# Performance work log

Measured on AMD Instinct MI355X. Metric: run time of the kernel, lower is better.

The kernel has to match this reference:

```python
import jax, jax.numpy as jnp
import numpy as np

D_M, D_K, D_V, HEADS = 1024, 64, 64, 16
B, S = 2, 2048


def setup_inputs() -> dict:
    key = jax.random.key(0)
    ks = jax.random.split(key, 5)
    x = jax.random.normal(ks[0], (B, S, D_M), dtype=jnp.float32)
    # per-head projection weights (original deep-copies one rand init per head;
    # we give each head independent weights, matching the per-head param structure)
    Wk = jax.random.uniform(ks[1], (HEADS, D_M, D_K), dtype=jnp.float32)
    Wq = jax.random.uniform(ks[2], (HEADS, D_M, D_K), dtype=jnp.float32)
    Wv = jax.random.uniform(ks[3], (HEADS, D_M, D_V), dtype=jnp.float32)
    Wo = jax.random.uniform(ks[4], (HEADS * D_V, D_M), dtype=jnp.float32)
    return {"x": x, "Wk": Wk, "Wq": Wq, "Wv": Wv, "Wo": Wo}


def reference(x, Wk, Wq, Wv, Wo):
    # per-head QKV projections, batched over heads: [B,H,S,d]
    q = jnp.einsum("bsm,hmk->bhsk", x, Wq)
    k = jnp.einsum("bsm,hmk->bhsk", x, Wk)
    v = jnp.einsum("bsm,hmv->bhsv", x, Wv)
    scale = 1.0 / jnp.sqrt(jnp.asarray(q.shape[-1], dtype=q.dtype))
    scores = jnp.einsum("bhsk,bhtk->bhst", q, k) * scale  # [B,H,S,S]
    attn = jax.nn.softmax(scores, axis=-1)
    ctx = jnp.einsum("bhst,bhtv->bhsv", attn, v)  # [B,H,S,d_v]
    # concat heads -> [B,S,H*d_v], then output projection
    ctx = jnp.transpose(ctx, (0, 2, 1, 3)).reshape(x.shape[0], x.shape[1], -1)
    return jnp.einsum("bsc,cm->bsm", ctx, Wo)
```

## Files before the change

kernel.cpp:

```cpp
#include <hip/hip_runtime.h>
#include <hip/hip_bf16.h>
#include <stdint.h>

#define DM   1024
#define DKV  64
#define HEADS 16
#define BATCH 2
#define SEQ  2048
#define BS   (BATCH*SEQ)
#define BHD  (BATCH*HEADS)

typedef __attribute__((ext_vector_type(8))) short bf16x8;
typedef __attribute__((ext_vector_type(4))) short bf16x4;
typedef __attribute__((ext_vector_type(4))) float f32x4;

__device__ inline unsigned fb(float f) { union { float f; unsigned u; } v; v.f = f; return v.u; }

__device__ inline unsigned short bf16_rtn(float f) {
  unsigned u = fb(f);
  unsigned r = u + 0x7fffu + ((u >> 16) & 1u);
  return (unsigned short)(r >> 16);
}
__device__ inline float bf16_to_f(unsigned short h) {
  union { unsigned u; float f; } v; v.u = ((unsigned)h) << 16; return v.f;
}
__device__ inline void split_bf16(float x, unsigned short& hi, unsigned short& lo) {
  hi = bf16_rtn(x);
  lo = bf16_rtn(x - bf16_to_f(hi));
}
__device__ inline unsigned pack2_bf16(float lo_elem, float hi_elem) {
  return __builtin_amdgcn_perm(fb(hi_elem) + 0x8000u, fb(lo_elem) + 0x8000u, 0x07060302u);
}

__device__ inline float fast_exp2(float x) {
#if __has_builtin(__builtin_amdgcn_exp2f)
  return __builtin_amdgcn_exp2f(x);
#else
  return exp2f(x);
#endif
}

__device__ inline f32x4 mfma16x16x16_bf16(bf16x4 a, bf16x4 b, f32x4 c) {
#if __has_builtin(__builtin_amdgcn_mfma_f32_16x16x16bf16_1k)
  return __builtin_amdgcn_mfma_f32_16x16x16bf16_1k(a, b, c, 0, 0, 0);
#else
  asm volatile("v_mfma_f32_16x16x16_bf16 %0, %1, %2, %0" : "+v"(c) : "v"(a), "v"(b));
  return c;
#endif
}

__device__ inline void stage16(const unsigned short* g, unsigned short* lds_base, int lane) {
#if __has_builtin(__builtin_amdgcn_global_load_lds)
  __builtin_amdgcn_global_load_lds((__attribute__((address_space(1))) void*)(g),
                                   (__attribute__((address_space(3))) void*)(lds_base),
                                   16, 0, 0);
#else
  *(bf16x8*)(lds_base + lane * 8) = *(const bf16x8*)g;
#endif
}

__device__ inline int swz(int row, int chunk) {
  return row * 64 + (((chunk ^ (row & 7)) & 7) << 3);
}

__global__ void cvt_x_split(const float* __restrict__ x,
                            unsigned short* __restrict__ xh, unsigned short* __restrict__ xl) {
  int i = (blockIdx.x * 256 + threadIdx.x) * 8;
  bf16x8 oh, ol;
  #pragma unroll
  for (int j = 0; j < 8; ++j) {
    unsigned short hi, lo;
    split_bf16(x[i + j], hi, lo);
    oh[j] = (short)hi; ol[j] = (short)lo;
  }
  *(bf16x8*)(xh + i) = oh;
  *(bf16x8*)(xl + i) = ol;
}

__global__ void pack_qkv_split(const float* __restrict__ Wq, const float* __restrict__ Wk,
                               const float* __restrict__ Wv,
                               unsigned short* __restrict__ Wh, unsigned short* __restrict__ Wl) {
  __shared__ float tile[64][65];
  int bid = blockIdx.x;
  int p = bid >> 8, h = (bid >> 4) & 15, mt = bid & 15;
  const float* W = (p == 0) ? Wq : (p == 1) ? Wk : Wv;
  const float* src = W + (size_t)h * (DM * DKV);
  int t = threadIdx.x;
  int m0 = mt * 64;
  #pragma unroll
  for (int pass = 0; pass < 16; ++pass) {
    int row = pass * 4 + (t >> 6), col = t & 63;
    tile[row][col] = src[(size_t)(m0 + row) * DKV + col];
  }
  __syncthreads();
  int cbase = p * 1024 + h * 64;
  #pragma unroll
  for (int pass = 0; pass < 16; ++pass) {
    int krow = pass * 4 + (t >> 6), mcol = t & 63;
    unsigned short hi, lo;
    split_bf16(tile[mcol][krow], hi, lo);
    size_t idx = (size_t)(cbase + krow) * DM + m0 + mcol;
    Wh[idx] = hi; Wl[idx] = lo;
  }
}

__global__ void pack_wo(const float* __restrict__ Wo, unsigned short* __restrict__ WoT) {
  __shared__ float tile[64][65];
  int ib = blockIdx.x >> 4, jb = blockIdx.x & 15;
  int t = threadIdx.x;
  #pragma unroll
  for (int pass = 0; pass < 16; ++pass) {
    int row = pass * 4 + (t >> 6), col = t & 63;
    tile[row][col] = Wo[(size_t)(ib * 64 + row) * DM + jb * 64 + col];
  }
  __syncthreads();
  #pragma unroll
  for (int pass = 0; pass < 16; ++pass) {
    int a = pass * 4 + (t >> 6), b = t & 63;
    WoT[(size_t)(jb * 64 + a) * DM + ib * 64 + b] = bf16_rtn(tile[b][a]);
  }
}

__global__ __launch_bounds__(256, 2)
void gemm_qk(const unsigned short* __restrict__ Ah, const unsigned short* __restrict__ Al,
             const unsigned short* __restrict__ Bh, const unsigned short* __restrict__ Bl,
             unsigned short* __restrict__ Qh, unsigned short* __restrict__ Ql,
             unsigned short* __restrict__ Kh, unsigned short* __restrict__ Kl) {
  __shared__ unsigned short AsH[128 * 32], AsL[128 * 32];
  __shared__ unsigned short BsH[128 * 32], BsL[128 * 32];
  const int tid = threadIdx.x;
  const int w = tid >> 6, lane = tid & 63;
  const int quad = lane >> 4, l16 = lane & 15;
  const int wm = w >> 1, wn = w & 1;
  const int bn = blockIdx.x, bm = blockIdx.y;

  f32x4 acc[4][4];
  #pragma unroll
  for (int i = 0; i < 4; ++i)
    #pragma unroll
    for (int j = 0; j < 4; ++j) acc[i][j] = (f32x4){0.f, 0.f, 0.f, 0.f};

  const int r4 = lane >> 2, c4 = lane & 3;
  const size_t offA = (size_t)(bm * 128 + w * 32 + r4) * DM + c4 * 8;
  const size_t offB = (size_t)(bn * 128 + w * 32 + r4) * DM + c4 * 8;
  unsigned short* lAh0 = AsH + (w * 32) * 32;      unsigned short* lAh1 = AsH + (w * 32 + 16) * 32;
  unsigned short* lAl0 = AsL + (w * 32) * 32;      unsigned short* lAl1 = AsL + (w * 32 + 16) * 32;
  unsigned short* lBh0 = BsH + (w * 32) * 32;      unsigned short* lBh1 = BsH + (w * 32 + 16) * 32;
  unsigned short* lBl0 = BsL + (w * 32) * 32;      unsigned short* lBl1 = BsL + (w * 32 + 16) * 32;

  for (int kk = 0; kk < DM / 32; ++kk) {
    stage16(Ah + offA + kk * 32,           lAh0, lane);
    stage16(Ah + offA + kk * 32 + 16 * DM, lAh1, lane);
    stage16(Al + offA + kk * 32,           lAl0, lane);
    stage16(Al + offA + kk * 32 + 16 * DM, lAl1, lane);
    stage16(Bh + offB + kk * 32,           lBh0, lane);
    stage16(Bh + offB + kk * 32 + 16 * DM, lBh1, lane);
    stage16(Bl + offB + kk * 32,           lBl0, lane);
    stage16(Bl + offB + kk * 32 + 16 * DM, lBl1, lane);
    asm volatile("s_waitcnt vmcnt(0)" ::: "memory");
    __syncthreads();
    bf16x8 afh[4], afl[4], bfh[4], bfl[4];
    #pragma unroll
    for (int mt = 0; mt < 4; ++mt) {
      afh[mt] = *(const bf16x8*)(AsH + (wm * 64 + mt * 16 + l16) * 32 + quad * 8);
      afl[mt] = *(const bf16x8*)(AsL + (wm * 64 + mt * 16 + l16) * 32 + quad * 8);
    }
    #pragma unroll
    for (int nt = 0; nt < 4; ++nt) {
      bfh[nt] = *(const bf16x8*)(BsH + (wn * 64 + nt * 16 + l16) * 32 + quad * 8);
      bfl[nt] = *(const bf16x8*)(BsL + (wn * 64 + nt * 16 + l16) * 32 + quad * 8);
    }
    #pragma unroll
    for (int mt = 0; mt < 4; ++mt)
      #pragma unroll
      for (int nt = 0; nt < 4; ++nt) {
        acc[mt][nt] = __builtin_amdgcn_mfma_f32_16x16x32_bf16(afh[mt], bfh[nt], acc[mt][nt], 0, 0, 0);
        acc[mt][nt] = __builtin_amdgcn_mfma_f32_16x16x32_bf16(afh[mt], bfl[nt], acc[mt][nt], 0, 0, 0);
        acc[mt][nt] = __builtin_amdgcn_mfma_f32_16x16x32_bf16(afl[mt], bfh[nt], acc[mt][nt], 0, 0, 0);
      }
    __syncthreads();
  }

  const float SCL = 0.18033688011112042f;
  #pragma unroll
  for (int mt = 0; mt < 4; ++mt) {
    int m_g = bm * 128 + wm * 64 + mt * 16 + quad * 4;
    #pragma unroll
    for (int nt = 0; nt < 4; ++nt) {
      int n_g = bn * 128 + wn * 64 + nt * 16 + l16;
      int p = n_g >> 10, h = (n_g >> 6) & 15, k = n_g & 63;
      #pragma unroll
      for (int r = 0; r < 4; ++r) {
        int row = m_g + r;
        int b = row >> 11, s = row & 2047;
        int bh = b * HEADS + h;
        float v = acc[mt][nt][r];
        size_t idx = ((size_t)(bh * SEQ + s)) * DKV + k;
        unsigned short hi, lo;
        if (p == 0) {
          split_bf16(v * SCL, hi, lo);
          Qh[idx] = hi; Ql[idx] = lo;
        } else {
          split_bf16(v, hi, lo);
          Kh[idx] = hi; Kl[idx] = lo;
        }
      }
    }
  }
}

__global__ __launch_bounds__(256, 2)
void gemm_v(const unsigned short* __restrict__ A, const unsigned short* __restrict__ Bt,
            unsigned short* __restrict__ Vt) {
  __shared__ unsigned short As[128 * 32];
  __shared__ unsigned short Bs[128 * 32];
  const int tid = threadIdx.x;
  const int w = tid >> 6, lane = tid & 63;
  const int quad = lane >> 4, l16 = lane & 15;
  const int wm = w >> 1, wn = w & 1;
  const int bn = blockIdx.x, bm = blockIdx.y;

  f32x4 acc[4][4];
  #pragma unroll
  for (int i = 0; i < 4; ++i)
    #pragma unroll
    for (int j = 0; j < 4; ++j) acc[i][j] = (f32x4){0.f, 0.f, 0.f, 0.f};

  const int r4 = lane >> 2, c4 = lane & 3;
  const unsigned short* gA0 = A  + (size_t)(bm * 128 + w * 32 + r4) * DM + c4 * 8;
  const unsigned short* gB0 = Bt + (size_t)(bn * 128 + w * 32 + r4) * DM + c4 * 8;
  unsigned short* lA0 = As + (w * 32) * 32;
  unsigned short* lA1 = As + (w * 32 + 16) * 32;
  unsigned short* lB0 = Bs + (w * 32) * 32;
  unsigned short* lB1 = Bs + (w * 32 + 16) * 32;

  for (int kk = 0; kk < DM / 32; ++kk) {
    stage16(gA0 + kk * 32,           lA0, lane);
    stage16(gA0 + kk * 32 + 16 * DM, lA1, lane);
    stage16(gB0 + kk * 32,           lB0, lane);
    stage16(gB0 + kk * 32 + 16 * DM, lB1, lane);
    asm volatile("s_waitcnt vmcnt(0)" ::: "memory");
    __syncthreads();
    bf16x8 af[4], bfr[4];
    #pragma unroll
    for (int mt = 0; mt < 4; ++mt)
      af[mt] = *(const bf16x8*)(As + (wm * 64 + mt * 16 + l16) * 32 + quad * 8);
    #pragma unroll
    for (int nt = 0; nt < 4; ++nt)
      bfr[nt] = *(const bf16x8*)(Bs + (wn * 64 + nt * 16 + l16) * 32 + quad * 8);
    #pragma unroll
    for (int mt = 0; mt < 4; ++mt)
      #pragma unroll
      for (int nt = 0; nt < 4; ++nt)
        acc[mt][nt] = __builtin_amdgcn_mfma_f32_16x16x32_bf16(af[mt], bfr[nt], acc[mt][nt], 0, 0, 0);
    __syncthreads();
  }

  #pragma unroll
  for (int mt = 0; mt < 4; ++mt) {
    int m_g = bm * 128 + wm * 64 + mt * 16 + quad * 4;
    #pragma unroll
    for (int nt = 0; nt < 4; ++nt) {
      int n_g = bn * 128 + wn * 64 + nt * 16 + l16;
      int h = n_g >> 6, k = n_g & 63;
      #pragma unroll
      for (int r = 0; r < 4; ++r) {
        int row = m_g + r;
        int b = row >> 11, s = row & 2047;
        int bh = b * HEADS + h;
        Vt[((size_t)(bh * DKV + k)) * SEQ + s] = bf16_rtn(acc[mt][nt][r]);
      }
    }
  }
}

__global__ __launch_bounds__(256, 2)
void flash(const unsigned short* __restrict__ Qh, const unsigned short* __restrict__ Ql,
           const unsigned short* __restrict__ Kh, const unsigned short* __restrict__ Kl,
           const unsigned short* __restrict__ Vt, unsigned short* __restrict__ ctx) {
  __shared__ unsigned short KtH[2][64 * 64], KtL[2][64 * 64], Vts[2][64 * 64];
  const int tid = threadIdx.x;
  const int w = tid >> 6, lane = tid & 63, quad = lane >> 4, l16 = lane & 15;
  const int bh = blockIdx.x;
  const int q0 = blockIdx.y * 128;

  bf16x8 qfh[2][2], qfl[2][2];
  #pragma unroll
  for (int qt = 0; qt < 2; ++qt) {
    int qrow = q0 + w * 32 + qt * 16 + l16;
    size_t base = ((size_t)(bh * SEQ + qrow)) * DKV + quad * 8;
    qfh[qt][0] = *(const bf16x8*)(Qh + base);
    qfh[qt][1] = *(const bf16x8*)(Qh + base + 32);
    qfl[qt][0] = *(const bf16x8*)(Ql + base);
    qfl[qt][1] = *(const bf16x8*)(Ql + base + 32);
  }

  float m_run[2] = {-1e30f, -1e30f};
  float l_run[2] = {0.f, 0.f};
  f32x4 acc[2][4];
  #pragma unroll
  for (int qt = 0; qt < 2; ++qt)
    #pragma unroll
    for (int vt = 0; vt < 4; ++vt) acc[qt][vt] = (f32x4){0.f, 0.f, 0.f, 0.f};

  const int srow = w * 16 + (lane >> 3);
  const int csrc = (lane & 7) ^ (lane >> 3);
  const unsigned short* kh_src = Kh + ((size_t)(bh * SEQ) + srow) * DKV + csrc * 8;
  const unsigned short* kl_src = Kl + ((size_t)(bh * SEQ) + srow) * DKV + csrc * 8;
  const unsigned short* v_src  = Vt + ((size_t)(bh * DKV) + srow) * SEQ + csrc * 8;

  #define STAGE(buf, kt0)                                                     \
    do {                                                                      \
      unsigned short* dH = &KtH[buf][(w * 16) * 64];                          \
      unsigned short* dL = &KtL[buf][(w * 16) * 64];                          \
      unsigned short* dV = &Vts[buf][(w * 16) * 64];                          \
      stage16(kh_src + (size_t)(kt0) * DKV,            dH,       lane);       \
      stage16(kh_src + (size_t)(kt0) * DKV + 8 * DKV,  dH + 512, lane);       \
      stage16(kl_src + (size_t)(kt0) * DKV,            dL,       lane);       \
      stage16(kl_src + (size_t)(kt0) * DKV + 8 * DKV,  dL + 512, lane);       \
      stage16(v_src  + (kt0),                          dV,       lane);       \
      stage16(v_src  + (kt0) + 8 * SEQ,                dV + 512, lane);       \
    } while (0)

  STAGE(0, 0);
  asm volatile("s_waitcnt vmcnt(0)" ::: "memory");
  __syncthreads();
  int cur = 0;

  for (int kt = 0; kt < SEQ / 64; ++kt) {
    if (kt + 1 < SEQ / 64) STAGE(cur ^ 1, (kt + 1) * 64);

    const unsigned short* kH = KtH[cur];
    const unsigned short* kL = KtL[cur];
    const unsigned short* vS = Vts[cur];

    f32x4 st[4][2];
    #pragma unroll
    for (int mt = 0; mt < 4; ++mt) {
      int rowA = mt * 16 + l16;
      bf16x8 kah0 = *(const bf16x8*)(kH + swz(rowA, quad));
      bf16x8 kah1 = *(const bf16x8*)(kH + swz(rowA, quad + 4));
      bf16x8 kal0 = *(const bf16x8*)(kL + swz(rowA, quad));
      bf16x8 kal1 = *(const bf16x8*)(kL + swz(rowA, quad + 4));
      #pragma unroll
      for (int qt = 0; qt < 2; ++qt) {
        f32x4 c = (f32x4){0.f, 0.f, 0.f, 0.f};
        c = __builtin_amdgcn_mfma_f32_16x16x32_bf16(kah0, qfh[qt][0], c, 0, 0, 0);
        c = __builtin_amdgcn_mfma_f32_16x16x32_bf16(kah1, qfh[qt][1], c, 0, 0, 0);
        c = __builtin_amdgcn_mfma_f32_16x16x32_bf16(kah0, qfl[qt][0], c, 0, 0, 0);
        c = __builtin_amdgcn_mfma_f32_16x16x32_bf16(kah1, qfl[qt][1], c, 0, 0, 0);
        c = __builtin_amdgcn_mfma_f32_16x16x32_bf16(kal0, qfh[qt][0], c, 0, 0, 0);
        c = __builtin_amdgcn_mfma_f32_16x16x32_bf16(kal1, qfh[qt][1], c, 0, 0, 0);
        st[mt][qt] = c;
      }
    }

    bf16x4 pb[2][4];
    #pragma unroll
    for (int qt = 0; qt < 2; ++qt) {
      float cm = -1e30f;
      #pragma unroll
      for (int mt = 0; mt < 4; ++mt)
        #pragma unroll
        for (int r = 0; r < 4; ++r) cm = fmaxf(cm, st[mt][qt][r]);
      cm = fmaxf(cm, __shfl_xor(cm, 16));
      cm = fmaxf(cm, __shfl_xor(cm, 32));
      bool upd = cm > m_run[qt];
      float mn = upd ? cm : m_run[qt];
      float ssum = 0.f;
      #pragma unroll
      for (int mt = 0; mt < 4; ++mt) {
        float p0 = fast_exp2(st[mt][qt][0] - mn);
        float p1 = fast_exp2(st[mt][qt][1] - mn);
        float p2 = fast_exp2(st[mt][qt][2] - mn);
        float p3 = fast_exp2(st[mt][qt][3] - mn);
        ssum += (p0 + p1) + (p2 + p3);
        union { bf16x4 v; unsigned u2[2]; } pk;
        pk.u2[0] = pack2_bf16(p0, p1);
        pk.u2[1] = pack2_bf16(p2, p3);
        pb[qt][mt] = pk.v;
      }
      ssum += __shfl_xor(ssum, 16);
      ssum += __shfl_xor(ssum, 32);
      if (__ballot(upd)) {
        float alpha = fast_exp2(m_run[qt] - mn);
        m_run[qt] = mn;
        l_run[qt] = l_run[qt] * alpha + ssum;
        #pragma unroll
        for (int vt = 0; vt < 4; ++vt) acc[qt][vt] = acc[qt][vt] * alpha;
      } else {
        l_run[qt] += ssum;
      }
    }

    #pragma unroll
    for (int vt = 0; vt < 4; ++vt) {
      #pragma unroll
      for (int mt = 0; mt < 4; ++mt) {
        int row = vt * 16 + l16;
        int addr = row * 64 + ((((mt * 2 + (quad >> 1)) ^ (row & 7)) & 7) << 3) + (quad & 1) * 4;
        bf16x4 va = *(const bf16x4*)(vS + addr);
        #pragma unroll
        for (int qt = 0; qt < 2; ++qt)
          acc[qt][vt] = mfma16x16x16_bf16(va, pb[qt][mt], acc[qt][vt]);
      }
    }

    asm volatile("s_waitcnt vmcnt(0)" ::: "memory");
    __syncthreads();
    cur ^= 1;
  }
  #undef STAGE

  int h = bh & 15, b = bh >> 4;
  #pragma unroll
  for (int qt = 0; qt < 2; ++qt) {
    float inv = 1.0f / l_run[qt];
    int bs = b * SEQ + q0 + w * 32 + qt * 16 + l16;
    #pragma unroll
    for (int vt = 0; vt < 4; ++vt) {
      union { bf16x4 v; unsigned u2[2]; } pk;
      pk.u2[0] = pack2_bf16(acc[qt][vt][0] * inv, acc[qt][vt][1] * inv);
      pk.u2[1] = pack2_bf16(acc[qt][vt][2] * inv, acc[qt][vt][3] * inv);
      *(bf16x4*)(ctx + (size_t)bs * DM + h * 64 + vt * 16 + quad * 4) = pk.v;
    }
  }
}

__global__ __launch_bounds__(256, 2)
void gemm_out(const unsigned short* __restrict__ A, const unsigned short* __restrict__ Bt,
              float* __restrict__ out) {
  __shared__ unsigned short As[128 * 32];
  __shared__ unsigned short Bs[128 * 32];
  const int tid = threadIdx.x;
  const int w = tid >> 6, lane = tid & 63;
  const int quad = lane >> 4, l16 = lane & 15;
  const int wm = w >> 1, wn = w & 1;
  const int bn = blockIdx.x, bm = blockIdx.y;

  f32x4 acc[4][4];
  #pragma unroll
  for (int i = 0; i < 4; ++i)
    #pragma unroll
    for (int j = 0; j < 4; ++j) acc[i][j] = (f32x4){0.f, 0.f, 0.f, 0.f};

  const int r4 = lane >> 2, c4 = lane & 3;
  const unsigned short* gA0 = A  + (size_t)(bm * 128 + w * 32 + r4) * DM + c4 * 8;
  const unsigned short* gB0 = Bt + (size_t)(bn * 128 + w * 32 + r4) * DM + c4 * 8;
  unsigned short* lA0 = As + (w * 32) * 32;
  unsigned short* lA1 = As + (w * 32 + 16) * 32;
  unsigned short* lB0 = Bs + (w * 32) * 32;
  unsigned short* lB1 = Bs + (w * 32 + 16) * 32;

  for (int kk = 0; kk < DM / 32; ++kk) {
    stage16(gA0 + kk * 32,           lA0, lane);
    stage16(gA0 + kk * 32 + 16 * DM, lA1, lane);
    stage16(gB0 + kk * 32,           lB0, lane);
    stage16(gB0 + kk * 32 + 16 * DM, lB1, lane);
    asm volatile("s_waitcnt vmcnt(0)" ::: "memory");
    __syncthreads();
    bf16x8 af[4], bfr[4];
    #pragma unroll
    for (int mt = 0; mt < 4; ++mt)
      af[mt] = *(const bf16x8*)(As + (wm * 64 + mt * 16 + l16) * 32 + quad * 8);
    #pragma unroll
    for (int nt = 0; nt < 4; ++nt)
      bfr[nt] = *(const bf16x8*)(Bs + (wn * 64 + nt * 16 + l16) * 32 + quad * 8);
    #pragma unroll
    for (int mt = 0; mt < 4; ++mt)
      #pragma unroll
      for (int nt = 0; nt < 4; ++nt)
        acc[mt][nt] = __builtin_amdgcn_mfma_f32_16x16x32_bf16(af[mt], bfr[nt], acc[mt][nt], 0, 0, 0);
    __syncthreads();
  }

  #pragma unroll
  for (int mt = 0; mt < 4; ++mt) {
    int m_g = bm * 128 + wm * 64 + mt * 16 + quad * 4;
    #pragma unroll
    for (int nt = 0; nt < 4; ++nt) {
      int n_g = bn * 128 + wn * 64 + nt * 16 + l16;
      #pragma unroll
      for (int r = 0; r < 4; ++r)
        out[(size_t)(m_g + r) * DM + n_g] = acc[mt][nt][r];
    }
  }
}

extern "C" void kernel_launch(void* const* d_in, const int* in_sizes, int n_in,
                              void* d_out, int out_size, void* d_ws, size_t ws_size,
                              hipStream_t stream) {
  const float* x  = (const float*)d_in[0];
  const float* Wk = (const float*)d_in[1];
  const float* Wq = (const float*)d_in[2];
  const float* Wv = (const float*)d_in[3];
  const float* Wo = (const float*)d_in[4];
  float* out = (float*)d_out;

  unsigned short* xh  = (unsigned short*)d_ws;
  unsigned short* xl  = xh  + (size_t)BS * DM;
  unsigned short* Wh  = xl  + (size_t)BS * DM;
  unsigned short* Wl  = Wh  + (size_t)3 * DM * DM;
  unsigned short* WoT = Wl  + (size_t)3 * DM * DM;
  unsigned short* Qh  = WoT + (size_t)DM * DM;
  unsigned short* Ql  = Qh  + (size_t)BHD * SEQ * DKV;
  unsigned short* Kh  = Ql  + (size_t)BHD * SEQ * DKV;
  unsigned short* Kl  = Kh  + (size_t)BHD * SEQ * DKV;
  unsigned short* Vtb = Kl  + (size_t)BHD * SEQ * DKV;
  unsigned short* ctx = Vtb + (size_t)BHD * SEQ * DKV;

  cvt_x_split<<<(BS * DM) / (256 * 8), 256, 0, stream>>>(x, xh, xl);
  pack_qkv_split<<<3 * 16 * 16, 256, 0, stream>>>(Wq, Wk, Wv, Wh, Wl);
  pack_wo<<<16 * 16, 256, 0, stream>>>(Wo, WoT);
  gemm_qk<<<dim3(16, 32), 256, 0, stream>>>(xh, xl, Wh, Wl, Qh, Ql, Kh, Kl);
  gemm_v<<<dim3(8, 32), 256, 0, stream>>>(xh, Wh + (size_t)2048 * DM, Vtb);
  flash<<<dim3(BHD, SEQ / 128), 256, 0, stream>>>(Qh, Ql, Kh, Kl, Vtb, ctx);
  gemm_out<<<dim3(8, 32), 256, 0, stream>>>(ctx, WoT, out);
}
```

Baseline: 272.1 us.

## Deepen GEMM K-tile to 64 with XOR-swizzled LDS, halve M-tile, add MFMA priority

The three projection GEMMs now stage 64-wide K slices per iteration instead of 32, which halves the number of barrier/wait round trips. LDS columns are XOR-swizzled per row to avoid bank conflicts on the fragment reads. gemm_v and gemm_out move to 64-row M tiles with twice as many blocks, to give more waves across the CUs. The flash kernel wraps its MFMA sections in s_setprio so the matrix work is favoured in wave scheduling. The cost is more LDS per block, especially in gemm_qk, which may lower occupancy.

New measurement: 242.0 us. -11.1%, faster.

```diff
diff --git a/kernel.cpp b/kernel.cpp
--- a/kernel.cpp
+++ b/kernel.cpp
@@ -126,8 +126,8 @@
              const unsigned short* __restrict__ Bh, const unsigned short* __restrict__ Bl,
              unsigned short* __restrict__ Qh, unsigned short* __restrict__ Ql,
              unsigned short* __restrict__ Kh, unsigned short* __restrict__ Kl) {
-  __shared__ unsigned short AsH[128 * 32], AsL[128 * 32];
-  __shared__ unsigned short BsH[128 * 32], BsL[128 * 32];
+  __shared__ unsigned short AsH[128 * 64], AsL[128 * 64];
+  __shared__ unsigned short BsH[128 * 64], BsL[128 * 64];
   const int tid = threadIdx.x;
   const int w = tid >> 6, lane = tid & 63;
   const int quad = lane >> 4, l16 = lane & 15;
@@ -140,44 +140,51 @@
     #pragma unroll
     for (int j = 0; j < 4; ++j) acc[i][j] = (f32x4){0.f, 0.f, 0.f, 0.f};
 
-  const int r4 = lane >> 2, c4 = lane & 3;
-  const size_t offA = (size_t)(bm * 128 + w * 32 + r4) * DM + c4 * 8;
-  const size_t offB = (size_t)(bn * 128 + w * 32 + r4) * DM + c4 * 8;
-  unsigned short* lAh0 = AsH + (w * 32) * 32;      unsigned short* lAh1 = AsH + (w * 32 + 16) * 32;
-  unsigned short* lAl0 = AsL + (w * 32) * 32;      unsigned short* lAl1 = AsL + (w * 32 + 16) * 32;
-  unsigned short* lBh0 = BsH + (w * 32) * 32;      unsigned short* lBh1 = BsH + (w * 32 + 16) * 32;
-  unsigned short* lBl0 = BsL + (w * 32) * 32;      unsigned short* lBl1 = BsL + (w * 32 + 16) * 32;
-
-  for (int kk = 0; kk < DM / 32; ++kk) {
-    stage16(Ah + offA + kk * 32,           lAh0, lane);
-    stage16(Ah + offA + kk * 32 + 16 * DM, lAh1, lane);
-    stage16(Al + offA + kk * 32,           lAl0, lane);
-    stage16(Al + offA + kk * 32 + 16 * DM, lAl1, lane);
-    stage16(Bh + offB + kk * 32,           lBh0, lane);
-    stage16(Bh + offB + kk * 32 + 16 * DM, lBh1, lane);
-    stage16(Bl + offB + kk * 32,           lBl0, lane);
-    stage16(Bl + offB + kk * 32 + 16 * DM, lBl1, lane);
+  const int r8 = lane >> 3, c8 = lane & 7;
+  const int cs = c8 ^ r8;
+  const size_t offA = (size_t)(bm * 128 + w * 32 + r8) * DM + cs * 8;
+  const size_t offB = (size_t)(bn * 128 + w * 32 + r8) * DM + cs * 8;
+
+  for (int kk = 0; kk < DM / 64; ++kk) {
+    #pragma unroll
+    for (int ps = 0; ps < 4; ++ps) {
+      unsigned short* dA = AsH + (w * 32 + ps * 8) * 64;
+      unsigned short* dAl = AsL + (w * 32 + ps * 8) * 64;
+      unsigned short* dB = BsH + (w * 32 + ps * 8) * 64;
+      unsigned short* dBl = BsL + (w * 32 + ps * 8) * 64;
+      stage16(Ah + offA + kk * 64 + ps * 8 * DM, dA,  lane);
+      stage16(Al + offA + kk * 64 + ps * 8 * DM, dAl, lane);
+      stage16(Bh + offB + kk * 64 + ps * 8 * DM, dB,  lane);
+      stage16(Bl + offB + kk * 64 + ps * 8 * DM, dBl, lane);
+    }
     asm volatile("s_waitcnt vmcnt(0)" ::: "memory");
     __syncthreads();
-    bf16x8 afh[4], afl[4], bfh[4], bfl[4];
-    #pragma unroll
-    for (int mt = 0; mt < 4; ++mt) {
-      afh[mt] = *(const bf16x8*)(AsH + (wm * 64 + mt * 16 + l16) * 32 + quad * 8);
-      afl[mt] = *(const bf16x8*)(AsL + (wm * 64 + mt * 16 + l16) * 32 + quad * 8);
-    }
-    #pragma unroll
-    for (int nt = 0; nt < 4; ++nt) {
-      bfh[nt] = *(const bf16x8*)(BsH + (wn * 64 + nt * 16 + l16) * 32 + quad * 8);
-      bfl[nt] = *(const bf16x8*)(BsL + (wn * 64 + nt * 16 + l16) * 32 + quad * 8);
-    }
-    #pragma unroll
-    for (int mt = 0; mt < 4; ++mt)
+    #pragma unroll
+    for (int ks = 0; ks < 2; ++ks) {
+      bf16x8 afh[4], afl[4], bfh[4], bfl[4];
+      #pragma unroll
+      for (int mt = 0; mt < 4; ++mt) {
+        int row = wm * 64 + mt * 16 + l16;
+        int ad = row * 64 + ((((ks * 4 + quad) ^ (row & 7)) & 7) << 3);
+        afh[mt] = *(const bf16x8*)(AsH + ad);
+        afl[mt] = *(const bf16x8*)(AsL + ad);
+      }
       #pragma unroll
       for (int nt = 0; nt < 4; ++nt) {
-        acc[mt][nt] = __builtin_amdgcn_mfma_f32_16x16x32_bf16(afh[mt], bfh[nt], acc[mt][nt], 0, 0, 0);
-        acc[mt][nt] = __builtin_amdgcn_mfma_f32_16x16x32_bf16(afh[mt], bfl[nt], acc[mt][nt], 0, 0, 0);
-        acc[mt][nt] = __builtin_amdgcn_mfma_f32_16x16x32_bf16(afl[mt], bfh[nt], acc[mt][nt], 0, 0, 0);
-      }
+        int row = wn * 64 + nt * 16 + l16;
+        int ad = row * 64 + ((((ks * 4 + quad) ^ (row & 7)) & 7) << 3);
+        bfh[nt] = *(const bf16x8*)(BsH + ad);
+        bfl[nt] = *(const bf16x8*)(BsL + ad);
+      }
+      #pragma unroll
+      for (int mt = 0; mt < 4; ++mt)
+        #pragma unroll
+        for (int nt = 0; nt < 4; ++nt) {
+          acc[mt][nt] = __builtin_amdgcn_mfma_f32_16x16x32_bf16(afh[mt], bfh[nt], acc[mt][nt], 0, 0, 0);
+          acc[mt][nt] = __builtin_amdgcn_mfma_f32_16x16x32_bf16(afh[mt], bfl[nt], acc[mt][nt], 0, 0, 0);
+          acc[mt][nt] = __builtin_amdgcn_mfma_f32_16x16x32_bf16(afl[mt], bfh[nt], acc[mt][nt], 0, 0, 0);
+        }
+    }
     __syncthreads();
   }
 
@@ -212,53 +219,59 @@
 __global__ __launch_bounds__(256, 2)
 void gemm_v(const unsigned short* __restrict__ A, const unsigned short* __restrict__ Bt,
             unsigned short* __restrict__ Vt) {
-  __shared__ unsigned short As[128 * 32];
-  __shared__ unsigned short Bs[128 * 32];
+  __shared__ unsigned short As[64 * 64];
+  __shared__ unsigned short Bs[128 * 64];
   const int tid = threadIdx.x;
   const int w = tid >> 6, lane = tid & 63;
   const int quad = lane >> 4, l16 = lane & 15;
   const int wm = w >> 1, wn = w & 1;
   const int bn = blockIdx.x, bm = blockIdx.y;
 
-  f32x4 acc[4][4];
-  #pragma unroll
-  for (int i = 0; i < 4; ++i)
+  f32x4 acc[2][4];
+  #pragma unroll
+  for (int i = 0; i < 2; ++i)
     #pragma unroll
     for (int j = 0; j < 4; ++j) acc[i][j] = (f32x4){0.f, 0.f, 0.f, 0.f};
 
-  const int r4 = lane >> 2, c4 = lane & 3;
-  const unsigned short* gA0 = A  + (size_t)(bm * 128 + w * 32 + r4) * DM + c4 * 8;
-  const unsigned short* gB0 = Bt + (size_t)(bn * 128 + w * 32 + r4) * DM + c4 * 8;
-  unsigned short* lA0 = As + (w * 32) * 32;
-  unsigned short* lA1 = As + (w * 32 + 16) * 32;
-  unsigned short* lB0 = Bs + (w * 32) * 32;
-  unsigned short* lB1 = Bs + (w * 32 + 16) * 32;
-
-  for (int kk = 0; kk < DM / 32; ++kk) {
-    stage16(gA0 + kk * 32,           lA0, lane);
-    stage16(gA0 + kk * 32 + 16 * DM, lA1, lane);
-    stage16(gB0 + kk * 32,           lB0, lane);
-    stage16(gB0 + kk * 32 + 16 * DM, lB1, lane);
+  const int r8 = lane >> 3, c8 = lane & 7;
+  const int cs = c8 ^ r8;
+  const size_t offA = (size_t)(bm * 64 + w * 16 + r8) * DM + cs * 8;
+  const size_t offB = (size_t)(bn * 128 + w * 32 + r8) * DM + cs * 8;
+
+  for (int kk = 0; kk < DM / 64; ++kk) {
+    #pragma unroll
+    for (int ps = 0; ps < 2; ++ps)
+      stage16(A + offA + kk * 64 + ps * 8 * DM, As + (w * 16 + ps * 8) * 64, lane);
+    #pragma unroll
+    for (int ps = 0; ps < 4; ++ps)
+      stage16(Bt + offB + kk * 64 + ps * 8 * DM, Bs + (w * 32 + ps * 8) * 64, lane);
     asm volatile("s_waitcnt vmcnt(0)" ::: "memory");
     __syncthreads();
-    bf16x8 af[4], bfr[4];
-    #pragma unroll
-    for (int mt = 0; mt < 4; ++mt)
-      af[mt] = *(const bf16x8*)(As + (wm * 64 + mt * 16 + l16) * 32 + quad * 8);
-    #pragma unroll
-    for (int nt = 0; nt < 4; ++nt)
-      bfr[nt] = *(const bf16x8*)(Bs + (wn * 64 + nt * 16 + l16) * 32 + quad * 8);
-    #pragma unroll
-    for (int mt = 0; mt < 4; ++mt)
-      #pragma unroll
-      for (int nt = 0; nt < 4; ++nt)
-        acc[mt][nt] = __builtin_amdgcn_mfma_f32_16x16x32_bf16(af[mt], bfr[nt], acc[mt][nt], 0, 0, 0);
-    __syncthreads();
-  }
-
-  #pragma unroll
-  for (int mt = 0; mt < 4; ++mt) {
-    int m_g = bm * 128 + wm * 64 + mt * 16 + quad * 4;
+    #pragma unroll
+    for (int ks = 0; ks < 2; ++ks) {
+      bf16x8 af[2], bfr[4];
+      #pragma unroll
+      for (int mt = 0; mt < 2; ++mt) {
+        int row = wm * 32 + mt * 16 + l16;
+        af[mt] = *(const bf16x8*)(As + row * 64 + ((((ks * 4 + quad) ^ (row & 7)) & 7) << 3));
+      }
+      #pragma unroll
+      for (int nt = 0; nt < 4; ++nt) {
+        int row = wn * 64 + nt * 16 + l16;
+        bfr[nt] = *(const bf16x8*)(Bs + row * 64 + ((((ks * 4 + quad) ^ (row & 7)) & 7) << 3));
+      }
+      #pragma unroll
+      for (int mt = 0; mt < 2; ++mt)
+        #pragma unroll
+        for (int nt = 0; nt < 4; ++nt)
+          acc[mt][nt] = __builtin_amdgcn_mfma_f32_16x16x32_bf16(af[mt], bfr[nt], acc[mt][nt], 0, 0, 0);
+    }
+    __syncthreads();
+  }
+
+  #pragma unroll
+  for (int mt = 0; mt < 2; ++mt) {
+    int m_g = bm * 64 + wm * 32 + mt * 16 + quad * 4;
     #pragma unroll
     for (int nt = 0; nt < 4; ++nt) {
       int n_g = bn * 128 + wn * 64 + nt * 16 + l16;
@@ -335,6 +348,7 @@
     const unsigned short* vS = Vts[cur];
 
     f32x4 st[4][2];
+    __builtin_amdgcn_s_setprio(1);
     #pragma unroll
     for (int mt = 0; mt < 4; ++mt) {
       int rowA = mt * 16 + l16;
@@ -354,6 +368,7 @@
         st[mt][qt] = c;
       }
     }
+    __builtin_amdgcn_s_setprio(0);
 
     bf16x4 pb[2][4];
     #pragma unroll
@@ -393,6 +408,7 @@
       }
     }
 
+    __builtin_amdgcn_s_setprio(1);
     #pragma unroll
     for (int vt = 0; vt < 4; ++vt) {
       #pragma unroll
@@ -405,6 +421,7 @@
           acc[qt][vt] = mfma16x16x16_bf16(va, pb[qt][mt], acc[qt][vt]);
       }
     }
+    __builtin_amdgcn_s_setprio(0);
 
     asm volatile("s_waitcnt vmcnt(0)" ::: "memory");
     __syncthreads();
@@ -430,53 +447,59 @@
 __global__ __launch_bounds__(256, 2)
 void gemm_out(const unsigned short* __restrict__ A, const unsigned short* __restrict__ Bt,
               float* __restrict__ out) {
-  __shared__ unsigned short As[128 * 32];
-  __shared__ unsigned short Bs[128 * 32];
+  __shared__ unsigned short As[64 * 64];
+  __shared__ unsigned short Bs[128 * 64];
   const int tid = threadIdx.x;
   const int w = tid >> 6, lane = tid & 63;
   const int quad = lane >> 4, l16 = lane & 15;
   const int wm = w >> 1, wn = w & 1;
   const int bn = blockIdx.x, bm = blockIdx.y;
 
-  f32x4 acc[4][4];
-  #pragma unroll
-  for (int i = 0; i < 4; ++i)
+  f32x4 acc[2][4];
+  #pragma unroll
+  for (int i = 0; i < 2; ++i)
     #pragma unroll
     for (int j = 0; j < 4; ++j) acc[i][j] = (f32x4){0.f, 0.f, 0.f, 0.f};
 
-  const int r4 = lane >> 2, c4 = lane & 3;
-  const unsigned short* gA0 = A  + (size_t)(bm * 128 + w * 32 + r4) * DM + c4 * 8;
-  const unsigned short* gB0 = Bt + (size_t)(bn * 128 + w * 32 + r4) * DM + c4 * 8;
-  unsigned short* lA0 = As + (w * 32) * 32;
-  unsigned short* lA1 = As + (w * 32 + 16) * 32;
-  unsigned short* lB0 = Bs + (w * 32) * 32;
-  unsigned short* lB1 = Bs + (w * 32 + 16) * 32;
-
-  for (int kk = 0; kk < DM / 32; ++kk) {
-    stage16(gA0 + kk * 32,           lA0, lane);
-    stage16(gA0 + kk * 32 + 16 * DM, lA1, lane);
-    stage16(gB0 + kk * 32,           lB0, lane);
-    stage16(gB0 + kk * 32 + 16 * DM, lB1, lane);
+  const int r8 = lane >> 3, c8 = lane & 7;
+  const int cs = c8 ^ r8;
+  const size_t offA = (size_t)(bm * 64 + w * 16 + r8) * DM + cs * 8;
+  const size_t offB = (size_t)(bn * 128 + w * 32 + r8) * DM + cs * 8;
+
+  for (int kk = 0; kk < DM / 64; ++kk) {
+    #pragma unroll
+    for (int ps = 0; ps < 2; ++ps)
+      stage16(A + offA + kk * 64 + ps * 8 * DM, As + (w * 16 + ps * 8) * 64, lane);
+    #pragma unroll
+    for (int ps = 0; ps < 4; ++ps)
+      stage16(Bt + offB + kk * 64 + ps * 8 * DM, Bs + (w * 32 + ps * 8) * 64, lane);
     asm volatile("s_waitcnt vmcnt(0)" ::: "memory");
     __syncthreads();
-    bf16x8 af[4], bfr[4];
-    #pragma unroll
-    for (int mt = 0; mt < 4; ++mt)
-      af[mt] = *(const bf16x8*)(As + (wm * 64 + mt * 16 + l16) * 32 + quad * 8);
-    #pragma unroll
-    for (int nt = 0; nt < 4; ++nt)
-      bfr[nt] = *(const bf16x8*)(Bs + (wn * 64 + nt * 16 + l16) * 32 + quad * 8);
-    #pragma unroll
-    for (int mt = 0; mt < 4; ++mt)
-      #pragma unroll
-      for (int nt = 0; nt < 4; ++nt)
-        acc[mt][nt] = __builtin_amdgcn_mfma_f32_16x16x32_bf16(af[mt], bfr[nt], acc[mt][nt], 0, 0, 0);
-    __syncthreads();
-  }
-
-  #pragma unroll
-  for (int mt = 0; mt < 4; ++mt) {
-    int m_g = bm * 128 + wm * 64 + mt * 16 + quad * 4;
+    #pragma unroll
+    for (int ks = 0; ks < 2; ++ks) {
+      bf16x8 af[2], bfr[4];
+      #pragma unroll
+      for (int mt = 0; mt < 2; ++mt) {
+        int row = wm * 32 + mt * 16 + l16;
+        af[mt] = *(const bf16x8*)(As + row * 64 + ((((ks * 4 + quad) ^ (row & 7)) & 7) << 3));
+      }
+      #pragma unroll
+      for (int nt = 0; nt < 4; ++nt) {
+        int row = wn * 64 + nt * 16 + l16;
+        bfr[nt] = *(const bf16x8*)(Bs + row * 64 + ((((ks * 4 + quad) ^ (row & 7)) & 7) << 3));
+      }
+      #pragma unroll
+      for (int mt = 0; mt < 2; ++mt)
+        #pragma unroll
+        for (int nt = 0; nt < 4; ++nt)
+          acc[mt][nt] = __builtin_amdgcn_mfma_f32_16x16x32_bf16(af[mt], bfr[nt], acc[mt][nt], 0, 0, 0);
+    }
+    __syncthreads();
+  }
+
+  #pragma unroll
+  for (int mt = 0; mt < 2; ++mt) {
+    int m_g = bm * 64 + wm * 32 + mt * 16 + quad * 4;
     #pragma unroll
     for (int nt = 0; nt < 4; ++nt) {
       int n_g = bn * 128 + wn * 64 + nt * 16 + l16;
@@ -513,7 +536,7 @@
   pack_qkv_split<<<3 * 16 * 16, 256, 0, stream>>>(Wq, Wk, Wv, Wh, Wl);
   pack_wo<<<16 * 16, 256, 0, stream>>>(Wo, WoT);
   gemm_qk<<<dim3(16, 32), 256, 0, stream>>>(xh, xl, Wh, Wl, Qh, Ql, Kh, Kl);
-  gemm_v<<<dim3(8, 32), 256, 0, stream>>>(xh, Wh + (size_t)2048 * DM, Vtb);
+  gemm_v<<<dim3(8, 64), 256, 0, stream>>>(xh, Wh + (size_t)2048 * DM, Vtb);
   flash<<<dim3(BHD, SEQ / 128), 256, 0, stream>>>(Qh, Ql, Kh, Kl, Vtb, ctx);
-  gemm_out<<<dim3(8, 32), 256, 0, stream>>>(ctx, WoT, out);
-}
+  gemm_out<<<dim3(8, 64), 256, 0, stream>>>(ctx, WoT, out);
+}
```
